# Kernel optimization log

Measured on AMD Instinct MI355X. Metric: run time of the kernel, lower is better.

The kernel has to match this reference:

```python
import jax, jax.numpy as jnp
import numpy as np

B, T, VOCAB_SZ, N_SPK = 64, 1024, 34, 128
D_TXT, D_SPK, H, N_MELS = 512, 64, 256, 80


def _lstm_params(key, in_dim, hid):
    k1, k2, k3, k4 = jax.random.split(key, 4)
    s = 1.0 / np.sqrt(hid)
    Wih = jax.random.uniform(k1, (4 * hid, in_dim), jnp.float32, -s, s)
    Whh = jax.random.uniform(k2, (4 * hid, hid), jnp.float32, -s, s)
    bih = jax.random.uniform(k3, (4 * hid,), jnp.float32, -s, s)
    bhh = jax.random.uniform(k4, (4 * hid,), jnp.float32, -s, s)
    return Wih, Whh, bih, bhh


def setup_inputs() -> dict:
    key = jax.random.key(0)
    ks = jax.random.split(key, 10)
    text_seq = jax.random.randint(ks[0], (B, T), 0, VOCAB_SZ)
    mel_spectrogram = jax.random.normal(ks[1], (B, T, N_MELS), jnp.float32)
    speaker_id = jax.random.randint(ks[2], (B,), 0, N_SPK)
    emb_text = jax.random.normal(ks[3], (VOCAB_SZ, D_TXT), jnp.float32)
    emb_text = emb_text.at[0].set(0.0)  # padding_idx=0
    emb_spk = jax.random.normal(ks[4], (N_SPK, D_SPK), jnp.float32)
    Wih_f, Whh_f, bih_f, bhh_f = _lstm_params(ks[5], D_TXT + D_SPK, H)
    Wih_b, Whh_b, bih_b, bhh_b = _lstm_params(ks[6], D_TXT + D_SPK, H)
    Wih_d, _Whh_d, bih_d, bhh_d = _lstm_params(ks[7], N_MELS + 2 * H, H)
    s = 1.0 / np.sqrt(H)
    Wfc = jax.random.uniform(ks[8], (N_MELS, H), jnp.float32, -s, s)
    bfc = jax.random.uniform(ks[9], (N_MELS,), jnp.float32, -s, s)
    return dict(text_seq=text_seq, mel_spectrogram=mel_spectrogram, speaker_id=speaker_id,
                emb_text=emb_text, emb_spk=emb_spk,
                Wih_f=Wih_f, Whh_f=Whh_f, bih_f=bih_f, bhh_f=bhh_f,
                Wih_b=Wih_b, Whh_b=Whh_b, bih_b=bih_b, bhh_b=bhh_b,
                Wih_d=Wih_d, bih_d=bih_d, bhh_d=bhh_d, Wfc=Wfc, bfc=bfc)


def _lstm_scan(xs, Wih, Whh, bih, bhh, reverse=False):
    # xs: [T, B, D] -> hs: [T, B, H] (PyTorch gate order i,f,g,o)
    nB, hid = xs.shape[1], Whh.shape[1]
    bias = bih + bhh
    def step(carry, x):
        h, c = carry
        g = x @ Wih.T + h @ Whh.T + bias
        i, f, gg, o = jnp.split(g, 4, axis=-1)
        c = jax.nn.sigmoid(f) * c + jax.nn.sigmoid(i) * jnp.tanh(gg)
        h = jax.nn.sigmoid(o) * jnp.tanh(c)
        return (h, c), h
    init = (jnp.zeros((nB, hid), xs.dtype), jnp.zeros((nB, hid), xs.dtype))
    _, hs = jax.lax.scan(step, init, xs, reverse=reverse)
    return hs


def reference(text_seq, mel_spectrogram, speaker_id, emb_text, emb_spk,
              Wih_f, Whh_f, bih_f, bhh_f, Wih_b, Whh_b, bih_b, bhh_b,
              Wih_d, bih_d, bhh_d, Wfc, bfc):
    text_embed = emb_text[text_seq]                       # [B, T, 512]
    spk = jnp.broadcast_to(emb_spk[speaker_id][:, None, :],
                           (text_seq.shape[0], text_seq.shape[1], emb_spk.shape[1]))
    enc_in = jnp.concatenate([text_embed, spk], axis=-1)  # [B, T, 576]
    xs = jnp.transpose(enc_in, (1, 0, 2))                 # time-major [T, B, 576]
    h_fwd = _lstm_scan(xs, Wih_f, Whh_f, bih_f, bhh_f)
    h_bwd = _lstm_scan(xs, Wih_b, Whh_b, bih_b, bhh_b, reverse=True)
    enc_out = jnp.concatenate([h_fwd, h_bwd], axis=-1)    # [T, B, 512]

    max_len = min(mel_spectrogram.shape[1], enc_out.shape[0])
    # Decoder: hidden state is reset (None) every step in the original, so
    # c = sigmoid(i)*tanh(g), h = sigmoid(o)*tanh(c); Whh contributes nothing.
    dbias = bih_d + bhh_d
    def dstep(prev_mel, e_t):
        x = jnp.concatenate([prev_mel, e_t], axis=-1)     # [B, 592]
        g = x @ Wih_d.T + dbias
        i, f, gg, o = jnp.split(g, 4, axis=-1)
        c = jax.nn.sigmoid(i) * jnp.tanh(gg)
        h = jax.nn.sigmoid(o) * jnp.tanh(c)
        out = h @ Wfc.T + bfc
        return out, out
    _, outs = jax.lax.scan(dstep, mel_spectrogram[:, 0, :], enc_out[: max_len - 1])
    return jnp.transpose(outs, (1, 0, 2))                 # [B, max_len-1, 80]
```

## Files before the change

kernel.cpp:

```cpp
#include <hip/hip_runtime.h>
#include <hip/hip_fp16.h>
#include <stdint.h>

#define T_SEQ 1024
#define NB    64
#define VOCAB 34
#define NSPK  128
#define DTXT  512
#define HID   256
#define NMEL  80
#define GROWS 1024
#define DROWS 768

typedef _Float16 f16;
typedef _Float16 f16x2 __attribute__((ext_vector_type(2)));

__device__ __forceinline__ float fdot2f(uint32_t a, uint32_t b, float c) {
  return __builtin_amdgcn_fdot2(__builtin_bit_cast(f16x2, a),
                                __builtin_bit_cast(f16x2, b), c, false);
}
__device__ __forceinline__ float sigm(float x) { return 1.0f / (1.0f + __expf(-x)); }
__device__ __forceinline__ float tanhf_fast(float x) {
  float e = __expf(2.0f * x);
  return 1.0f - 2.0f / (e + 1.0f);
}


__global__ void k_tp(const float* __restrict__ Wf, const float* __restrict__ Wb,
                     const float* __restrict__ emb_text, float* __restrict__ TP) {
  int blk = blockIdx.x; int dir = blk / VOCAB; int v = blk - dir * VOCAB;
  const float* W = dir ? Wb : Wf;
  const float* e = emb_text + (size_t)v * DTXT;
  for (int r = threadIdx.x; r < GROWS; r += 256) {
    const float* wr = W + (size_t)r * 576;
    float a0 = 0, a1 = 0, a2 = 0, a3 = 0;
    for (int d = 0; d < DTXT; d += 4) {
      a0 += e[d] * wr[d];     a1 += e[d+1] * wr[d+1];
      a2 += e[d+2] * wr[d+2]; a3 += e[d+3] * wr[d+3];
    }
    TP[(size_t)(dir * VOCAB + v) * GROWS + r] = (a0 + a1) + (a2 + a3);
  }
}

__global__ void k_sp(const float* __restrict__ Wf, const float* __restrict__ Wb,
                     const float* __restrict__ bihf, const float* __restrict__ bhhf,
                     const float* __restrict__ bihb, const float* __restrict__ bhhb,
                     const float* __restrict__ emb_spk, float* __restrict__ SP) {
  int blk = blockIdx.x; int dir = blk >> 7; int s = blk & 127;
  const float* W  = dir ? Wb : Wf;
  const float* bi = dir ? bihb : bihf;
  const float* bh = dir ? bhhb : bhhf;
  const float* e  = emb_spk + (size_t)s * 64;
  for (int r = threadIdx.x; r < GROWS; r += 256) {
    const float* wr = W + (size_t)r * 576 + 512;
    float acc = bi[r] + bh[r];
    for (int d = 0; d < 64; ++d) acc += e[d] * wr[d];
    SP[(size_t)(dir * NSPK + s) * GROWS + r] = acc;
  }
}

__global__ void k_whh(const float* __restrict__ Whhf, const float* __restrict__ Whhb,
                      f16* __restrict__ WhhH) {
  int idx = blockIdx.x * 256 + threadIdx.x;
  if (idx < 2 * GROWS * HID) {
    int dir = idx >> 18; int rem = idx & (GROWS * HID - 1);
    WhhH[idx] = (f16)(dir ? Whhb[rem] : Whhf[rem]);
  }
}

__global__ void k_decw(const float* __restrict__ Wih_d, const float* __restrict__ bih_d,
                       const float* __restrict__ bhh_d,
                       f16* __restrict__ WmH, f16* __restrict__ WdH, float* __restrict__ dbias) {
  int r = blockIdx.x;
  int src = (r < 256) ? r : (r + 256);
  const float* w = Wih_d + (size_t)src * 592;
  for (int k = threadIdx.x; k < 592; k += 256) {
    float v = w[k];
    if (k < 80) WmH[(size_t)r * 80 + k] = (f16)v;
    else        WdH[(size_t)r * 512 + (k - 80)] = (f16)v;
  }
  if (threadIdx.x == 0) dbias[r] = bih_d[src] + bhh_d[src];
}

__global__ void k_misc(const float* __restrict__ Wfc, f16* __restrict__ WfcH) {
  int idx = blockIdx.x * 256 + threadIdx.x;
  if (idx < NMEL * HID) WfcH[idx] = (f16)Wfc[idx];
}

__launch_bounds__(512)
__attribute__((amdgpu_waves_per_eu(2, 2)))
__global__ void k_enc(const int* __restrict__ text_seq, const int* __restrict__ speaker_id,
                      const float* __restrict__ TP, const float* __restrict__ SP,
                      const uint32_t* __restrict__ WhhH_dw,
                      f16* __restrict__ Hh) {
  __shared__ __align__(16) uint4 wtail[16 * 512];
  __shared__ __align__(16) uint32_t hbuf[2][128];
  __shared__ float pp[4][256];
  __shared__ int tseq[T_SEQ];

  int wg = blockIdx.x;
  int dir = wg >> 6, b = wg & 63;
  int tid = threadIdx.x;
  int u = tid & 255, kh = tid >> 8;

  uint4 w0[12], w1[12], w2[12], w3[12];
  {
    const uint4* p0 = (const uint4*)(WhhH_dw + ((size_t)(dir << 10) + u      ) * 128 + (kh << 6));
    const uint4* p1 = (const uint4*)(WhhH_dw + ((size_t)(dir << 10) + u + 256) * 128 + (kh << 6));
    const uint4* p2 = (const uint4*)(WhhH_dw + ((size_t)(dir << 10) + u + 512) * 128 + (kh << 6));
    const uint4* p3 = (const uint4*)(WhhH_dw + ((size_t)(dir << 10) + u + 768) * 128 + (kh << 6));
    #pragma unroll
    for (int i = 0; i < 12; ++i) { w0[i] = p0[i]; w1[i] = p1[i]; w2[i] = p2[i]; w3[i] = p3[i]; }
    #pragma unroll
    for (int j = 0; j < 4; ++j) {
      wtail[(0 * 4 + j) * 512 + tid] = p0[12 + j];
      wtail[(1 * 4 + j) * 512 + tid] = p1[12 + j];
      wtail[(2 * 4 + j) * 512 + tid] = p2[12 + j];
      wtail[(3 * 4 + j) * 512 + tid] = p3[12 + j];
    }
  }
  for (int i = tid; i < T_SEQ; i += 512) tseq[i] = text_seq[b * T_SEQ + i];
  if (tid < 128) hbuf[0][tid] = 0u;
  float sp0 = 0, sp1 = 0, sp2 = 0, sp3 = 0;
  if (kh == 0) {
    int spk = speaker_id[b];
    sp0 = SP[(size_t)(dir * NSPK + spk) * GROWS + u];
    sp1 = SP[(size_t)(dir * NSPK + spk) * GROWS + u + 256];
    sp2 = SP[(size_t)(dir * NSPK + spk) * GROWS + u + 512];
    sp3 = SP[(size_t)(dir * NSPK + spk) * GROWS + u + 768];
  }
  const float* TPd = TP + (size_t)dir * VOCAB * GROWS;
  float c_state = 0.0f;
  __syncthreads();

  float x0 = 0, x1 = 0, x2 = 0, x3 = 0;
  if (kh == 0) {
    int v = tseq[dir ? (T_SEQ - 1) : 0];
    x0 = TPd[(size_t)v * GROWS + u];
    x1 = TPd[(size_t)v * GROWS + u + 256];
    x2 = TPd[(size_t)v * GROWS + u + 512];
    x3 = TPd[(size_t)v * GROWS + u + 768];
  }

  float h_keep = 0.0f; int t_keep = 0;
  for (int n = 0; n < T_SEQ; ++n) {
    int t = dir ? (T_SEQ - 1 - n) : n;
    float xn0 = 0, xn1 = 0, xn2 = 0, xn3 = 0;
    if (kh == 0) {
      if (n > 0)
        Hh[((size_t)(dir * T_SEQ + t_keep) * NB + b) * HID + u] = (f16)h_keep;
      int tn = dir ? (T_SEQ - 2 - n) : (n + 1);
      tn = tn < 0 ? 0 : (tn > T_SEQ - 1 ? T_SEQ - 1 : tn);
      int vn = tseq[tn];
      xn0 = TPd[(size_t)vn * GROWS + u];
      xn1 = TPd[(size_t)vn * GROWS + u + 256];
      xn2 = TPd[(size_t)vn * GROWS + u + 512];
      xn3 = TPd[(size_t)vn * GROWS + u + 768];
    }

    float i0 = 0, i1 = 0, f0 = 0, f1 = 0, g0 = 0, g1 = 0, o0 = 0, o1 = 0;
    const uint4* h4 = ((const uint4*)hbuf[n & 1]) + (kh << 4);
    #pragma unroll
    for (int c = 0; c < 12; ++c) {
      uint4 hv = h4[c];
      i0 = fdot2f(w0[c].x, hv.x, i0); f0 = fdot2f(w1[c].x, hv.x, f0);
      g0 = fdot2f(w2[c].x, hv.x, g0); o0 = fdot2f(w3[c].x, hv.x, o0);
      i1 = fdot2f(w0[c].y, hv.y, i1); f1 = fdot2f(w1[c].y, hv.y, f1);
      g1 = fdot2f(w2[c].y, hv.y, g1); o1 = fdot2f(w3[c].y, hv.y, o1);
      i0 = fdot2f(w0[c].z, hv.z, i0); f0 = fdot2f(w1[c].z, hv.z, f0);
      g0 = fdot2f(w2[c].z, hv.z, g0); o0 = fdot2f(w3[c].z, hv.z, o0);
      i1 = fdot2f(w0[c].w, hv.w, i1); f1 = fdot2f(w1[c].w, hv.w, f1);
      g1 = fdot2f(w2[c].w, hv.w, g1); o1 = fdot2f(w3[c].w, hv.w, o1);
    }
    #pragma unroll
    for (int j = 0; j < 4; ++j) {
      uint4 hv = h4[12 + j];
      uint4 t0v = wtail[(0 * 4 + j) * 512 + tid];
      uint4 t1v = wtail[(1 * 4 + j) * 512 + tid];
      uint4 t2v = wtail[(2 * 4 + j) * 512 + tid];
      uint4 t3v = wtail[(3 * 4 + j) * 512 + tid];
      i0 = fdot2f(t0v.x, hv.x, i0); f0 = fdot2f(t1v.x, hv.x, f0);
      g0 = fdot2f(t2v.x, hv.x, g0); o0 = fdot2f(t3v.x, hv.x, o0);
      i1 = fdot2f(t0v.y, hv.y, i1); f1 = fdot2f(t1v.y, hv.y, f1);
      g1 = fdot2f(t2v.y, hv.y, g1); o1 = fdot2f(t3v.y, hv.y, o1);
      i0 = fdot2f(t0v.z, hv.z, i0); f0 = fdot2f(t1v.z, hv.z, f0);
      g0 = fdot2f(t2v.z, hv.z, g0); o0 = fdot2f(t3v.z, hv.z, o0);
      i1 = fdot2f(t0v.w, hv.w, i1); f1 = fdot2f(t1v.w, hv.w, f1);
      g1 = fdot2f(t2v.w, hv.w, g1); o1 = fdot2f(t3v.w, hv.w, o1);
    }
    if (kh == 1) {
      pp[0][u] = i0 + i1;
      pp[1][u] = f0 + f1;
      pp[2][u] = g0 + g1;
      pp[3][u] = o0 + o1;
    }
    __syncthreads();

    if (kh == 0) {
      float gi = (i0 + i1) + pp[0][u] + x0 + sp0;
      float gf = (f0 + f1) + pp[1][u] + x1 + sp1;
      float gg = (g0 + g1) + pp[2][u] + x2 + sp2;
      float go = (o0 + o1) + pp[3][u] + x3 + sp3;
      c_state = sigm(gf) * c_state + sigm(gi) * tanhf_fast(gg);
      float h = sigm(go) * tanhf_fast(c_state);
      ((f16*)hbuf[(n + 1) & 1])[u] = (f16)h;
      h_keep = h; t_keep = t;
      x0 = xn0; x1 = xn1; x2 = xn2; x3 = xn3;
    }
    __syncthreads();
  }
  if (kh == 0)
    Hh[((size_t)(dir * T_SEQ + t_keep) * NB + b) * HID + u] = (f16)h_keep;
}

__launch_bounds__(256, 4)
__global__ void k_eproj(const uint32_t* __restrict__ Hdw, const uint32_t* __restrict__ WdH_dw,
                        const float* __restrict__ dbias, f16* __restrict__ E) {
  __shared__ __align__(16) uint32_t Asm[64][68];
  __shared__ __align__(16) uint32_t Wsm[64][68];
  int nt = blockIdx.x % 12;
  int t  = blockIdx.x / 12;
  int n0 = nt * 64;
  int tid = threadIdx.x;
  int i = tid & 15, j = tid >> 4;
  float acc[4][4] = {};

  for (int ch = 0; ch < 4; ++ch) {
    int dirc = ch >> 1, koff = (ch & 1) * 64;
    {
      int bb = tid >> 2, p = tid & 3;
      const uint32_t* asrc = Hdw + ((size_t)(dirc * T_SEQ + t) * NB + bb) * 128 + koff + p * 4;
      const uint32_t* wsrc = WdH_dw + (size_t)(n0 + bb) * 256 + ch * 64 + p * 4;
      #pragma unroll
      for (int q = 0; q < 4; ++q) {
        *(uint4*)(&Asm[bb][p * 4 + q * 16]) = *(const uint4*)(asrc + q * 16);
        *(uint4*)(&Wsm[bb][p * 4 + q * 16]) = *(const uint4*)(wsrc + q * 16);
      }
    }
    __syncthreads();
    #pragma unroll
    for (int kc = 0; kc < 16; ++kc) {
      uint4 av[4], wv4[4];
      #pragma unroll
      for (int r = 0; r < 4; ++r) av[r]  = *(const uint4*)&Asm[i + 16 * r][kc * 4];
      #pragma unroll
      for (int s = 0; s < 4; ++s) wv4[s] = *(const uint4*)&Wsm[j + 16 * s][kc * 4];
      #pragma unroll
      for (int r = 0; r < 4; ++r)
        #pragma unroll
        for (int s = 0; s < 4; ++s) {
          acc[r][s] = fdot2f(av[r].x, wv4[s].x, acc[r][s]);
          acc[r][s] = fdot2f(av[r].y, wv4[s].y, acc[r][s]);
          acc[r][s] = fdot2f(av[r].z, wv4[s].z, acc[r][s]);
          acc[r][s] = fdot2f(av[r].w, wv4[s].w, acc[r][s]);
        }
    }
    __syncthreads();
  }
  #pragma unroll
  for (int r = 0; r < 4; ++r)
    #pragma unroll
    for (int s = 0; s < 4; ++s) {
      int m = i + 16 * r;
      int n = n0 + j + 16 * s;
      E[((size_t)t * NB + m) * DROWS + n] = (f16)(acc[r][s] + dbias[n]);
    }
}

__launch_bounds__(256, 1)
__global__ void k_dec(const float* __restrict__ mel, const f16* __restrict__ E,
                      const uint32_t* __restrict__ WmH_dw, const uint32_t* __restrict__ WfcH_dw,
                      const float* __restrict__ bfc, float* __restrict__ out) {
  __shared__ __align__(16) uint32_t pm[40];
  __shared__ __align__(16) uint32_t h_sm[128];
  __shared__ float partial[80][2];
  __shared__ __align__(16) uint4 Ebuf[2][16 * 96];

  int b = blockIdx.x;
  int tid = threadIdx.x;

  uint4 wm0[10], wm1[10], wm2[10];
  {
    const uint4* p0 = (const uint4*)(WmH_dw + (size_t)(tid      ) * 40);
    const uint4* p1 = (const uint4*)(WmH_dw + (size_t)(tid + 256) * 40);
    const uint4* p2 = (const uint4*)(WmH_dw + (size_t)(tid + 512) * 40);
    #pragma unroll
    for (int k = 0; k < 10; ++k) { wm0[k] = p0[k]; wm1[k] = p1[k]; wm2[k] = p2[k]; }
  }
  int fr = (tid < 160) ? (tid >> 1) : 0;
  int fs = tid & 1;
  uint4 wfc[16];
  {
    const uint4* wp = (const uint4*)(WfcH_dw + (size_t)fr * 128 + fs * 64);
    #pragma unroll
    for (int q = 0; q < 16; ++q) wfc[q] = wp[q];
  }
  float bfcv = bfc[tid < NMEL ? tid : 0];
  if (tid < 40) {
    float m0 = mel[(size_t)b * T_SEQ * NMEL + 2 * tid];
    float m1 = mel[(size_t)b * T_SEQ * NMEL + 2 * tid + 1];
    f16x2 v; v[0] = (f16)m0; v[1] = (f16)m1;
    pm[tid] = __builtin_bit_cast(uint32_t, v);
  }

  int srow = tid >> 4, scol = tid & 15;
  {
    int rr = srow; if (rr > T_SEQ - 2) rr = T_SEQ - 2;
    const uint4* src = (const uint4*)(E + ((size_t)rr * NB + b) * DROWS);
    #pragma unroll
    for (int k = 0; k < 6; ++k)
      Ebuf[0][srow * 96 + scol + 16 * k] = src[scol + 16 * k];
  }
  __syncthreads();

  float o_keep = 0.0f;
  for (int t = 0; t < T_SEQ - 1; ++t) {
    int w = t >> 4, s = t & 15;
    if (t > 0 && tid < NMEL)
      out[((size_t)b * (T_SEQ - 1) + (t - 1)) * NMEL + tid] = o_keep;
    uint4 st[6];
    bool do_stage = (s == 0) && (w < ((T_SEQ - 2) >> 4));
    if (do_stage) {
      int rr = (w + 1) * 16 + srow; if (rr > T_SEQ - 2) rr = T_SEQ - 2;
      const uint4* src = (const uint4*)(E + ((size_t)rr * NB + b) * DROWS);
      #pragma unroll
      for (int k = 0; k < 6; ++k) st[k] = src[scol + 16 * k];
    }

    const f16* Erow = (const f16*)&Ebuf[w & 1][s * 96];
    float a0 = (float)Erow[tid];
    float a1 = (float)Erow[tid + 256];
    float a2 = (float)Erow[tid + 512];
    const uint4* pm4 = (const uint4*)pm;
    #pragma unroll
    for (int k = 0; k < 10; ++k) {
      uint4 hp = pm4[k];
      a0 = fdot2f(wm0[k].x, hp.x, a0); a1 = fdot2f(wm1[k].x, hp.x, a1); a2 = fdot2f(wm2[k].x, hp.x, a2);
      a0 = fdot2f(wm0[k].y, hp.y, a0); a1 = fdot2f(wm1[k].y, hp.y, a1); a2 = fdot2f(wm2[k].y, hp.y, a2);
      a0 = fdot2f(wm0[k].z, hp.z, a0); a1 = fdot2f(wm1[k].z, hp.z, a1); a2 = fdot2f(wm2[k].z, hp.z, a2);
      a0 = fdot2f(wm0[k].w, hp.w, a0); a1 = fdot2f(wm1[k].w, hp.w, a1); a2 = fdot2f(wm2[k].w, hp.w, a2);
    }
    float cc = sigm(a0) * tanhf_fast(a1);
    float h  = sigm(a2) * tanhf_fast(cc);
    ((f16*)h_sm)[tid] = (f16)h;
    __syncthreads();

    if (tid < 160) {
      const uint4* hrow = (const uint4*)&h_sm[fs * 64];
      float s0 = 0, s1 = 0, s2 = 0, s3 = 0;
      #pragma unroll
      for (int q = 0; q < 16; ++q) {
        uint4 hq = hrow[q];
        s0 = fdot2f(wfc[q].x, hq.x, s0); s1 = fdot2f(wfc[q].y, hq.y, s1);
        s2 = fdot2f(wfc[q].z, hq.z, s2); s3 = fdot2f(wfc[q].w, hq.w, s3);
      }
      partial[fr][fs] = (s0 + s1) + (s2 + s3);
    }
    if (do_stage) {
      #pragma unroll
      for (int k = 0; k < 6; ++k)
        Ebuf[(w + 1) & 1][srow * 96 + scol + 16 * k] = st[k];
    }
    __syncthreads();

    if (tid < NMEL) {
      float o = partial[tid][0] + partial[tid][1] + bfcv;
      o_keep = o;
      ((f16*)pm)[tid] = (f16)o;
    }
    __syncthreads();
  }
  if (tid < NMEL)
    out[((size_t)b * (T_SEQ - 1) + (T_SEQ - 2)) * NMEL + tid] = o_keep;
}

extern "C" void kernel_launch(void* const* d_in, const int* in_sizes, int n_in,
                              void* d_out, int out_size, void* d_ws, size_t ws_size,
                              hipStream_t stream) {
  const int*   text_seq   = (const int*)d_in[0];
  const float* mel        = (const float*)d_in[1];
  const int*   speaker_id = (const int*)d_in[2];
  const float* emb_text   = (const float*)d_in[3];
  const float* emb_spk    = (const float*)d_in[4];
  const float* Wih_f = (const float*)d_in[5];
  const float* Whh_f = (const float*)d_in[6];
  const float* bih_f = (const float*)d_in[7];
  const float* bhh_f = (const float*)d_in[8];
  const float* Wih_b = (const float*)d_in[9];
  const float* Whh_b = (const float*)d_in[10];
  const float* bih_b = (const float*)d_in[11];
  const float* bhh_b = (const float*)d_in[12];
  const float* Wih_d = (const float*)d_in[13];
  const float* bih_d = (const float*)d_in[14];
  const float* bhh_d = (const float*)d_in[15];
  const float* Wfc   = (const float*)d_in[16];
  const float* bfc   = (const float*)d_in[17];
  float* out = (float*)d_out;

  char* base = (char*)d_ws;
  size_t off = 0;
  auto take = [&](size_t n) -> char* {
    off = (off + 255) & ~(size_t)255;
    char* r = base + off;
    off += n;
    return r;
  };
  float*        TP    = (float*)take((size_t)2 * VOCAB * GROWS * 4);
  float*        SP    = (float*)take((size_t)2 * NSPK * GROWS * 4);
  f16*          WhhH  = (f16*)take((size_t)2 * GROWS * HID * 2);
  f16*          WmH   = (f16*)take((size_t)DROWS * 80 * 2);
  f16*          WdH   = (f16*)take((size_t)DROWS * 512 * 2);
  f16*          WfcH  = (f16*)take((size_t)NMEL * HID * 2);
  float*        dbias = (float*)take((size_t)DROWS * 4);
  f16*          Hh    = (f16*)take((size_t)2 * T_SEQ * NB * HID * 2);
  f16*          E     = (f16*)take((size_t)(T_SEQ - 1) * NB * DROWS * 2);
  if (off > ws_size) return;

  k_tp  <<<2 * VOCAB, 256, 0, stream>>>(Wih_f, Wih_b, emb_text, TP);
  k_sp  <<<2 * NSPK, 256, 0, stream>>>(Wih_f, Wih_b, bih_f, bhh_f, bih_b, bhh_b, emb_spk, SP);
  k_whh <<<2048, 256, 0, stream>>>(Whh_f, Whh_b, WhhH);
  k_decw<<<DROWS, 256, 0, stream>>>(Wih_d, bih_d, bhh_d, WmH, WdH, dbias);
  k_misc<<<80, 256, 0, stream>>>(Wfc, WfcH);
  k_enc <<<128, 512, 0, stream>>>(text_seq, speaker_id, TP, SP,
                                  (const uint32_t*)WhhH, Hh);
  k_eproj<<<(T_SEQ - 1) * 12, 256, 0, stream>>>((const uint32_t*)Hh,
                                                (const uint32_t*)WdH, dbias, E);
  k_dec <<<NB, 256, 0, stream>>>(mel, E, (const uint32_t*)WmH,
                                 (const uint32_t*)WfcH, bfc, out);
}
```

Baseline: 3.394 ms.

## Split decoder K across 512 threads and offload encoder h stores to idle half

Result: slower. 3.498 ms (+3.1%).

```diff
diff --git a/kernel.cpp b/kernel.cpp
--- a/kernel.cpp
+++ b/kernel.cpp
@@ -142,13 +142,9 @@
     x3 = TPd[(size_t)v * GROWS + u + 768];
   }
 
-  float h_keep = 0.0f; int t_keep = 0;
   for (int n = 0; n < T_SEQ; ++n) {
-    int t = dir ? (T_SEQ - 1 - n) : n;
     float xn0 = 0, xn1 = 0, xn2 = 0, xn3 = 0;
     if (kh == 0) {
-      if (n > 0)
-        Hh[((size_t)(dir * T_SEQ + t_keep) * NB + b) * HID + u] = (f16)h_keep;
       int tn = dir ? (T_SEQ - 2 - n) : (n + 1);
       tn = tn < 0 ? 0 : (tn > T_SEQ - 1 ? T_SEQ - 1 : tn);
       int vn = tseq[tn];
@@ -156,10 +152,43 @@
       xn1 = TPd[(size_t)vn * GROWS + u + 256];
       xn2 = TPd[(size_t)vn * GROWS + u + 512];
       xn3 = TPd[(size_t)vn * GROWS + u + 768];
+    } else if (n > 0) {
+      int t_prev = dir ? (T_SEQ - n) : (n - 1);
+      f16 hv = ((const f16*)hbuf[n & 1])[u];
+      Hh[((size_t)(dir * T_SEQ + t_prev) * NB + b) * HID + u] = hv;
     }
 
     float i0 = 0, i1 = 0, f0 = 0, f1 = 0, g0 = 0, g1 = 0, o0 = 0, o1 = 0;
     const uint4* h4 = ((const uint4*)hbuf[n & 1]) + (kh << 4);
+
+    #pragma unroll
+    for (int jj = 0; jj < 2; ++jj) {
+      uint4 hva = h4[12 + 2 * jj], hvb = h4[13 + 2 * jj];
+      uint4 ta0 = wtail[(0 * 4 + 2 * jj) * 512 + tid];
+      uint4 tb0 = wtail[(1 * 4 + 2 * jj) * 512 + tid];
+      uint4 tc0 = wtail[(2 * 4 + 2 * jj) * 512 + tid];
+      uint4 td0 = wtail[(3 * 4 + 2 * jj) * 512 + tid];
+      uint4 ta1 = wtail[(0 * 4 + 2 * jj + 1) * 512 + tid];
+      uint4 tb1 = wtail[(1 * 4 + 2 * jj + 1) * 512 + tid];
+      uint4 tc1 = wtail[(2 * 4 + 2 * jj + 1) * 512 + tid];
+      uint4 td1 = wtail[(3 * 4 + 2 * jj + 1) * 512 + tid];
+      i0 = fdot2f(ta0.x, hva.x, i0); f0 = fdot2f(tb0.x, hva.x, f0);
+      g0 = fdot2f(tc0.x, hva.x, g0); o0 = fdot2f(td0.x, hva.x, o0);
+      i1 = fdot2f(ta0.y, hva.y, i1); f1 = fdot2f(tb0.y, hva.y, f1);
+      g1 = fdot2f(tc0.y, hva.y, g1); o1 = fdot2f(td0.y, hva.y, o1);
+      i0 = fdot2f(ta0.z, hva.z, i0); f0 = fdot2f(tb0.z, hva.z, f0);
+      g0 = fdot2f(tc0.z, hva.z, g0); o0 = fdot2f(td0.z, hva.z, o0);
+      i1 = fdot2f(ta0.w, hva.w, i1); f1 = fdot2f(tb0.w, hva.w, f1);
+      g1 = fdot2f(tc0.w, hva.w, g1); o1 = fdot2f(td0.w, hva.w, o1);
+      i0 = fdot2f(ta1.x, hvb.x, i0); f0 = fdot2f(tb1.x, hvb.x, f0);
+      g0 = fdot2f(tc1.x, hvb.x, g0); o0 = fdot2f(td1.x, hvb.x, o0);
+      i1 = fdot2f(ta1.y, hvb.y, i1); f1 = fdot2f(tb1.y, hvb.y, f1);
+      g1 = fdot2f(tc1.y, hvb.y, g1); o1 = fdot2f(td1.y, hvb.y, o1);
+      i0 = fdot2f(ta1.z, hvb.z, i0); f0 = fdot2f(tb1.z, hvb.z, f0);
+      g0 = fdot2f(tc1.z, hvb.z, g0); o0 = fdot2f(td1.z, hvb.z, o0);
+      i1 = fdot2f(ta1.w, hvb.w, i1); f1 = fdot2f(tb1.w, hvb.w, f1);
+      g1 = fdot2f(tc1.w, hvb.w, g1); o1 = fdot2f(td1.w, hvb.w, o1);
+    }
     #pragma unroll
     for (int c = 0; c < 12; ++c) {
       uint4 hv = h4[c];
@@ -172,22 +201,6 @@
       i1 = fdot2f(w0[c].w, hv.w, i1); f1 = fdot2f(w1[c].w, hv.w, f1);
       g1 = fdot2f(w2[c].w, hv.w, g1); o1 = fdot2f(w3[c].w, hv.w, o1);
     }
-    #pragma unroll
-    for (int j = 0; j < 4; ++j) {
-      uint4 hv = h4[12 + j];
-      uint4 t0v = wtail[(0 * 4 + j) * 512 + tid];
-      uint4 t1v = wtail[(1 * 4 + j) * 512 + tid];
-      uint4 t2v = wtail[(2 * 4 + j) * 512 + tid];
-      uint4 t3v = wtail[(3 * 4 + j) * 512 + tid];
-      i0 = fdot2f(t0v.x, hv.x, i0); f0 = fdot2f(t1v.x, hv.x, f0);
-      g0 = fdot2f(t2v.x, hv.x, g0); o0 = fdot2f(t3v.x, hv.x, o0);
-      i1 = fdot2f(t0v.y, hv.y, i1); f1 = fdot2f(t1v.y, hv.y, f1);
-      g1 = fdot2f(t2v.y, hv.y, g1); o1 = fdot2f(t3v.y, hv.y, o1);
-      i0 = fdot2f(t0v.z, hv.z, i0); f0 = fdot2f(t1v.z, hv.z, f0);
-      g0 = fdot2f(t2v.z, hv.z, g0); o0 = fdot2f(t3v.z, hv.z, o0);
-      i1 = fdot2f(t0v.w, hv.w, i1); f1 = fdot2f(t1v.w, hv.w, f1);
-      g1 = fdot2f(t2v.w, hv.w, g1); o1 = fdot2f(t3v.w, hv.w, o1);
-    }
     if (kh == 1) {
       pp[0][u] = i0 + i1;
       pp[1][u] = f0 + f1;
@@ -204,13 +217,15 @@
       c_state = sigm(gf) * c_state + sigm(gi) * tanhf_fast(gg);
       float h = sigm(go) * tanhf_fast(c_state);
       ((f16*)hbuf[(n + 1) & 1])[u] = (f16)h;
-      h_keep = h; t_keep = t;
       x0 = xn0; x1 = xn1; x2 = xn2; x3 = xn3;
     }
     __syncthreads();
   }
-  if (kh == 0)
-    Hh[((size_t)(dir * T_SEQ + t_keep) * NB + b) * HID + u] = (f16)h_keep;
+  if (kh == 1) {
+    int t_prev = dir ? 0 : (T_SEQ - 1);
+    f16 hv = ((const f16*)hbuf[T_SEQ & 1])[u];
+    Hh[((size_t)(dir * T_SEQ + t_prev) * NB + b) * HID + u] = hv;
+  }
 }
 
 __launch_bounds__(256, 4)
@@ -267,33 +282,36 @@
     }
 }
 
-__launch_bounds__(256, 1)
+__launch_bounds__(512)
+__attribute__((amdgpu_waves_per_eu(2, 2)))
 __global__ void k_dec(const float* __restrict__ mel, const f16* __restrict__ E,
                       const uint32_t* __restrict__ WmH_dw, const uint32_t* __restrict__ WfcH_dw,
                       const float* __restrict__ bfc, float* __restrict__ out) {
   __shared__ __align__(16) uint32_t pm[40];
   __shared__ __align__(16) uint32_t h_sm[128];
-  __shared__ float partial[80][2];
+  __shared__ float pp[3][256];
+  __shared__ float partial[80][4];
   __shared__ __align__(16) uint4 Ebuf[2][16 * 96];
 
   int b = blockIdx.x;
   int tid = threadIdx.x;
-
-  uint4 wm0[10], wm1[10], wm2[10];
+  int u = tid & 255, kh = tid >> 8;
+
+  uint4 wm0[5], wm1[5], wm2[5];
   {
-    const uint4* p0 = (const uint4*)(WmH_dw + (size_t)(tid      ) * 40);
-    const uint4* p1 = (const uint4*)(WmH_dw + (size_t)(tid + 256) * 40);
-    const uint4* p2 = (const uint4*)(WmH_dw + (size_t)(tid + 512) * 40);
-    #pragma unroll
-    for (int k = 0; k < 10; ++k) { wm0[k] = p0[k]; wm1[k] = p1[k]; wm2[k] = p2[k]; }
-  }
-  int fr = (tid < 160) ? (tid >> 1) : 0;
-  int fs = tid & 1;
-  uint4 wfc[16];
+    const uint4* p0 = (const uint4*)(WmH_dw + (size_t)(u      ) * 40) + kh * 5;
+    const uint4* p1 = (const uint4*)(WmH_dw + (size_t)(u + 256) * 40) + kh * 5;
+    const uint4* p2 = (const uint4*)(WmH_dw + (size_t)(u + 512) * 40) + kh * 5;
+    #pragma unroll
+    for (int k = 0; k < 5; ++k) { wm0[k] = p0[k]; wm1[k] = p1[k]; wm2[k] = p2[k]; }
+  }
+  int fr = (tid < 320) ? (tid >> 2) : 0;
+  int q  = tid & 3;
+  uint4 wfc[8];
   {
-    const uint4* wp = (const uint4*)(WfcH_dw + (size_t)fr * 128 + fs * 64);
-    #pragma unroll
-    for (int q = 0; q < 16; ++q) wfc[q] = wp[q];
+    const uint4* wp = (const uint4*)(WfcH_dw + (size_t)fr * 128) + q * 8;
+    #pragma unroll
+    for (int k = 0; k < 8; ++k) wfc[k] = wp[k];
   }
   float bfcv = bfc[tid < NMEL ? tid : 0];
   if (tid < 40) {
@@ -303,13 +321,12 @@
     pm[tid] = __builtin_bit_cast(uint32_t, v);
   }
 
-  int srow = tid >> 4, scol = tid & 15;
+  int srow = tid >> 5, scol = tid & 31;
   {
-    int rr = srow; if (rr > T_SEQ - 2) rr = T_SEQ - 2;
-    const uint4* src = (const uint4*)(E + ((size_t)rr * NB + b) * DROWS);
-    #pragma unroll
-    for (int k = 0; k < 6; ++k)
-      Ebuf[0][srow * 96 + scol + 16 * k] = src[scol + 16 * k];
+    const uint4* src = (const uint4*)(E + ((size_t)srow * NB + b) * DROWS);
+    Ebuf[0][srow * 96 + scol     ] = src[scol];
+    Ebuf[0][srow * 96 + scol + 32] = src[scol + 32];
+    Ebuf[0][srow * 96 + scol + 64] = src[scol + 64];
   }
   __syncthreads();
 
@@ -318,53 +335,59 @@
     int w = t >> 4, s = t & 15;
     if (t > 0 && tid < NMEL)
       out[((size_t)b * (T_SEQ - 1) + (t - 1)) * NMEL + tid] = o_keep;
-    uint4 st[6];
-    bool do_stage = (s == 0) && (w < ((T_SEQ - 2) >> 4));
+    uint4 st0, st1, st2;
+    bool do_stage = (s == 0) && (w < 63);
     if (do_stage) {
       int rr = (w + 1) * 16 + srow; if (rr > T_SEQ - 2) rr = T_SEQ - 2;
       const uint4* src = (const uint4*)(E + ((size_t)rr * NB + b) * DROWS);
-      #pragma unroll
-      for (int k = 0; k < 6; ++k) st[k] = src[scol + 16 * k];
-    }
-
-    const f16* Erow = (const f16*)&Ebuf[w & 1][s * 96];
-    float a0 = (float)Erow[tid];
-    float a1 = (float)Erow[tid + 256];
-    float a2 = (float)Erow[tid + 512];
-    const uint4* pm4 = (const uint4*)pm;
-    #pragma unroll
-    for (int k = 0; k < 10; ++k) {
+      st0 = src[scol]; st1 = src[scol + 32]; st2 = src[scol + 64];
+    }
+
+    float a0 = 0, a1 = 0, a2 = 0;
+    const uint4* pm4 = ((const uint4*)pm) + kh * 5;
+    #pragma unroll
+    for (int k = 0; k < 5; ++k) {
       uint4 hp = pm4[k];
       a0 = fdot2f(wm0[k].x, hp.x, a0); a1 = fdot2f(wm1[k].x, hp.x, a1); a2 = fdot2f(wm2[k].x, hp.x, a2);
       a0 = fdot2f(wm0[k].y, hp.y, a0); a1 = fdot2f(wm1[k].y, hp.y, a1); a2 = fdot2f(wm2[k].y, hp.y, a2);
       a0 = fdot2f(wm0[k].z, hp.z, a0); a1 = fdot2f(wm1[k].z, hp.z, a1); a2 = fdot2f(wm2[k].z, hp.z, a2);
       a0 = fdot2f(wm0[k].w, hp.w, a0); a1 = fdot2f(wm1[k].w, hp.w, a1); a2 = fdot2f(wm2[k].w, hp.w, a2);
     }
-    float cc = sigm(a0) * tanhf_fast(a1);
-    float h  = sigm(a2) * tanhf_fast(cc);
-    ((f16*)h_sm)[tid] = (f16)h;
-    __syncthreads();
-
-    if (tid < 160) {
-      const uint4* hrow = (const uint4*)&h_sm[fs * 64];
+    if (kh == 1) { pp[0][u] = a0; pp[1][u] = a1; pp[2][u] = a2; }
+    __syncthreads();
+
+    if (kh == 0) {
+      const f16* Erow = (const f16*)&Ebuf[w & 1][s * 96];
+      float gi = a0 + pp[0][u] + (float)Erow[u];
+      float gg = a1 + pp[1][u] + (float)Erow[u + 256];
+      float go = a2 + pp[2][u] + (float)Erow[u + 512];
+      float cc = sigm(gi) * tanhf_fast(gg);
+      float h  = sigm(go) * tanhf_fast(cc);
+      ((f16*)h_sm)[u] = (f16)h;
+    }
+    if (do_stage) {
+      Ebuf[(w + 1) & 1][srow * 96 + scol     ] = st0;
+      Ebuf[(w + 1) & 1][srow * 96 + scol + 32] = st1;
+      Ebuf[(w + 1) & 1][srow * 96 + scol + 64] = st2;
+    }
+    __syncthreads();
+
+    if (tid < 320) {
+      const uint4* hrow = ((const uint4*)h_sm) + q * 8;
       float s0 = 0, s1 = 0, s2 = 0, s3 = 0;
       #pragma unroll
-      for (int q = 0; q < 16; ++q) {
-        uint4 hq = hrow[q];
-        s0 = fdot2f(wfc[q].x, hq.x, s0); s1 = fdot2f(wfc[q].y, hq.y, s1);
-        s2 = fdot2f(wfc[q].z, hq.z, s2); s3 = fdot2f(wfc[q].w, hq.w, s3);
+      for (int kk = 0; kk < 8; ++kk) {
+        uint4 hq = hrow[kk];
+        s0 = fdot2f(wfc[kk].x, hq.x, s0); s1 = fdot2f(wfc[kk].y, hq.y, s1);
+        s2 = fdot2f(wfc[kk].z, hq.z, s2); s3 = fdot2f(wfc[kk].w, hq.w, s3);
       }
-      partial[fr][fs] = (s0 + s1) + (s2 + s3);
-    }
-    if (do_stage) {
-      #pragma unroll
-      for (int k = 0; k < 6; ++k)
-        Ebuf[(w + 1) & 1][srow * 96 + scol + 16 * k] = st[k];
+      partial[fr][q] = (s0 + s1) + (s2 + s3);
     }
     __syncthreads();
 
     if (tid < NMEL) {
-      float o = partial[tid][0] + partial[tid][1] + bfcv;
+      float o = ((partial[tid][0] + partial[tid][1]) +
+                 (partial[tid][2] + partial[tid][3])) + bfcv;
       o_keep = o;
       ((f16*)pm)[tid] = (f16)o;
     }
@@ -425,6 +448,6 @@
                                   (const uint32_t*)WhhH, Hh);
   k_eproj<<<(T_SEQ - 1) * 12, 256, 0, stream>>>((const uint32_t*)Hh,
                                                 (const uint32_t*)WdH, dbias, E);
-  k_dec <<<NB, 256, 0, stream>>>(mel, E, (const uint32_t*)WmH,
+  k_dec <<<NB, 512, 0, stream>>>(mel, E, (const uint32_t*)WmH,
                                  (const uint32_t*)WfcH, bfc, out);
 }
```
